# Kernel tuning notes

Hardware: AMD Instinct MI355X
Metric: run time of the kernel (lower is better)

## Reference

```python
import jax, jax.numpy as jnp
import numpy as np

K = 8        # num_heads
D = 32       # out_dim per head
KD = K * D   # 256
IN = 256     # in_dim
N_AUTHOR = 50000
N_PAPER = 50000
E = 400000
SLOPE = 0.2  # LeakyReLU negative slope


def setup_inputs() -> dict:
    key = jax.random.key(0)
    ks = jax.random.split(key, 26)
    f32 = jnp.float32
    nrm = lambda k, shp, s=0.05: jax.random.normal(k, shp, f32) * s
    ridx = lambda k, n: jax.random.randint(k, (E,), 0, n, jnp.int32)
    return {
        # node features
        "feats_author": nrm(ks[0], (N_AUTHOR, IN), 1.0),
        "feats_paper": nrm(ks[1], (N_PAPER, IN), 1.0),
        # micro (per node type) projection + attention vectors
        "W_micro_author": nrm(ks[2], (IN, KD)),
        "W_micro_paper": nrm(ks[3], (IN, KD)),
        "attn_micro_author": nrm(ks[4], (K, 2 * D)),
        "attn_micro_paper": nrm(ks[5], (K, 2 * D)),
        # macro: node projection per ntype, relation projection per etype
        "W_macro_node_author": nrm(ks[6], (IN, KD)),
        "W_macro_node_paper": nrm(ks[7], (IN, KD)),
        "W_macro_rel_writes": nrm(ks[8], (KD, KD)),
        "W_macro_rel_written_by": nrm(ks[9], (KD, KD)),
        "W_macro_rel_cites": nrm(ks[10], (KD, KD)),
        "attn_macro": nrm(ks[11], (K, 2 * D)),
        # residual
        "W_res_author": nrm(ks[12], (IN, KD)),
        "b_res_author": jnp.zeros((KD,), f32),
        "W_res_paper": nrm(ks[13], (IN, KD)),
        "b_res_paper": jnp.zeros((KD,), f32),
        "res_w_author": jax.random.uniform(ks[14], (1,), f32),
        "res_w_paper": jax.random.uniform(ks[15], (1,), f32),
        # graph: author-writes->paper, paper-written_by->author, paper-cites->paper
        "writes_src": ridx(ks[16], N_AUTHOR),
        "writes_dst": ridx(ks[17], N_PAPER),
        "written_by_src": ridx(ks[18], N_PAPER),
        "written_by_dst": ridx(ks[19], N_AUTHOR),
        "cites_src": ridx(ks[20], N_PAPER),
        "cites_dst": ridx(ks[21], N_PAPER),
    }


def _edge_softmax(e, dst, n_dst):
    # softmax over incoming edges of each destination node; e: (E, K)
    m = jax.ops.segment_max(e, dst, num_segments=n_dst)
    ex = jnp.exp(e - m[dst])
    s = jax.ops.segment_sum(ex, dst, num_segments=n_dst)
    return ex / s[dst]


def _micro(h_src, h_dst, W_s, W_d, attn, src, dst, n_dst):
    # GAT-style per-relation message passing (MicroConv, dropout=0 eval)
    fs = (h_src @ W_s).reshape(-1, K, D)   # (N_src, K, D)
    fd = (h_dst @ W_d).reshape(-1, K, D)   # (N_dst, K, D)
    el = (fs * attn[:, :D]).sum(-1)        # (N_src, K)
    er = (fd * attn[:, D:]).sum(-1)        # (N_dst, K)
    e = jax.nn.leaky_relu(el[src] + er[dst], SLOPE)  # (E, K)
    a = _edge_softmax(e, dst, n_dst)
    ft = jax.ops.segment_sum(fs[src] * a[:, :, None], dst, num_segments=n_dst)
    return jax.nn.relu(ft.reshape(n_dst, KD))


def reference(feats_author, feats_paper, W_micro_author, W_micro_paper,
              attn_micro_author, attn_micro_paper, W_macro_node_author,
              W_macro_node_paper, W_macro_rel_writes, W_macro_rel_written_by,
              W_macro_rel_cites, attn_macro, W_res_author, b_res_author,
              W_res_paper, b_res_paper, res_w_author, res_w_paper,
              writes_src, writes_dst, written_by_src, written_by_dst,
              cites_src, cites_dst):
    # --- micro conv per relation; fc_src/fc_dst keyed by node type, attn by src type ---
    r_writes = _micro(feats_author, feats_paper, W_micro_author, W_micro_paper,
                      attn_micro_author, writes_src, writes_dst, N_PAPER)
    r_written_by = _micro(feats_paper, feats_author, W_micro_paper, W_micro_author,
                          attn_micro_paper, written_by_src, written_by_dst, N_AUTHOR)
    r_cites = _micro(feats_paper, feats_paper, W_micro_paper, W_micro_paper,
                     attn_micro_paper, cites_src, cites_dst, N_PAPER)

    # --- macro conv: relation-level projection ---
    rf_writes = (r_writes @ W_macro_rel_writes).reshape(-1, K, D)
    rf_written_by = (r_written_by @ W_macro_rel_written_by).reshape(-1, K, D)
    rf_cites = (r_cites @ W_macro_rel_cites).reshape(-1, K, D)

    # author: single incoming relation -> passthrough
    out_author = rf_written_by.reshape(-1, KD)

    # paper: two incoming relations -> semantic attention fusion
    node_paper = (feats_paper @ W_macro_node_paper).reshape(-1, K, D)
    rf = jnp.stack([rf_writes, rf_cites], axis=0)          # (R=2, N, K, D)
    node_b = jnp.broadcast_to(node_paper, rf.shape)
    cat = jnp.concatenate([node_b, rf], axis=-1)           # (R, N, K, 2D)
    scores = jax.nn.leaky_relu((attn_macro * cat).sum(-1, keepdims=True), SLOPE)
    scores = jax.nn.softmax(scores, axis=0)                # over relations
    out_paper = (scores * rf).sum(0).reshape(-1, KD)

    # --- gated residual ---
    a_a = jax.nn.sigmoid(res_w_author)
    a_p = jax.nn.sigmoid(res_w_paper)
    out_author = a_a * out_author + (1 - a_a) * (feats_author @ W_res_author + b_res_author)
    out_paper = a_p * out_paper + (1 - a_p) * (feats_paper @ W_res_paper + b_res_paper)
    return out_author, out_paper
```

## Files before the change

kernel.cpp:

```cpp
#include <hip/hip_runtime.h>
#include <hip/hip_bf16.h>
#include <type_traits>


#define N_AUTHOR 50000
#define N_PAPER  50000
#define NEDGE    400000
#define KDIM     256
#define NHEAD    8
#define SLOPE    0.2f

#define BUCK_W   512
#define NBUCK    98
#define SBUF_CAP 6144

#define CSR_STRIDE 450004
#define CSR_GSRC   50004

using bf16 = __hip_bfloat16;
typedef __attribute__((ext_vector_type(8))) short short8;
typedef __attribute__((ext_vector_type(4))) float float4e;

__device__ __forceinline__ float us2f(unsigned short u) {
    return __uint_as_float(((unsigned int)u) << 16);
}
__device__ __forceinline__ float fin(float v) {
    return (((__float_as_uint(v) >> 23) & 0xFF) != 0xFF) ? v : 0.f;
}
__device__ __forceinline__ unsigned short f2bu(float f) {
    f = fin(f);
    bf16 h = __float2bfloat16(f);
    return *reinterpret_cast<unsigned short*>(&h);
}
__device__ __forceinline__ int clampi(int v, int hi) {
    return v < 0 ? 0 : (v >= hi ? hi - 1 : v);
}

__global__ void fill_marker(float* __restrict__ out, int total, float c)
{
    int i = blockIdx.x * blockDim.x + threadIdx.x;
    if (i < total) out[i] = c;
}

__device__ __forceinline__ float sel8(const float p[8], int j)
{
    float q = p[0];
    q = j == 1 ? p[1] : q; q = j == 2 ? p[2] : q; q = j == 3 ? p[3] : q;
    q = j == 4 ? p[4] : q; q = j == 5 ? p[5] : q; q = j == 6 ? p[6] : q;
    q = j == 7 ? p[7] : q;
    return q;
}

__device__ __forceinline__ float head_reduce(float p[8], int lane)
{
    #pragma unroll
    for (int h = 0; h < 8; ++h) {
        p[h] += __shfl_xor(p[h], 1);
        p[h] += __shfl_xor(p[h], 2);
        p[h] += __shfl_xor(p[h], 4);
    }
    float q = sel8(p, lane & 7);
    q += __shfl_xor(q, 8);
    q += __shfl_xor(q, 16);
    q += __shfl_xor(q, 32);
    return q;
}

__global__ void prep_bt(const float* __restrict__ W, bf16* __restrict__ BT)
{
    int n = blockIdx.x, k = threadIdx.x;
    reinterpret_cast<unsigned short*>(BT)[n * KDIM + k] = f2bu(W[k * KDIM + n]);
}

template<int MODE, typename TA>
__global__ __launch_bounds__(256) void mfma_gemm(
    const TA* __restrict__ A, const bf16* __restrict__ BT, int M,
    void* __restrict__ Cout,
    const float* __restrict__ bias, const bf16* __restrict__ other,
    const float* __restrict__ gate,
    const bf16* __restrict__ rfw, const float* __restrict__ sc_w,
    const float* __restrict__ sc_c)
{
    __shared__ short As[128 * 40];
    __shared__ short Bs[128 * 40];
    const int tid = threadIdx.x;
    const int lane = tid & 63, wave = tid >> 6;
    const int wm = wave >> 1, wn = wave & 1;
    const int rowBase = blockIdx.y * 128;
    const int colBase = blockIdx.x * 128;

    float4e acc[4][4];
    #pragma unroll
    for (int i = 0; i < 4; ++i)
        #pragma unroll
        for (int j = 0; j < 4; ++j) {
            float4e z = {0.f, 0.f, 0.f, 0.f};
            acc[i][j] = z;
        }

    const int srow = tid >> 2;
    const int sq = (tid & 3) << 3;

    for (int kt = 0; kt < KDIM; kt += 32) {
        #pragma unroll
        for (int p = 0; p < 2; ++p) {
            int r = srow + p * 64;
            int gr = rowBase + r;
            short8 v = {0, 0, 0, 0, 0, 0, 0, 0};
            if (gr < M) {
                if constexpr (std::is_same<TA, float>::value) {
                    const float* ap = A + (size_t)gr * KDIM + kt + sq;
                    float4 x = *reinterpret_cast<const float4*>(ap);
                    float4 y = *reinterpret_cast<const float4*>(ap + 4);
                    v[0] = (short)f2bu(x.x); v[1] = (short)f2bu(x.y);
                    v[2] = (short)f2bu(x.z); v[3] = (short)f2bu(x.w);
                    v[4] = (short)f2bu(y.x); v[5] = (short)f2bu(y.y);
                    v[6] = (short)f2bu(y.z); v[7] = (short)f2bu(y.w);
                } else {
                    v = *reinterpret_cast<const short8*>(
                        reinterpret_cast<const short*>(A) + (size_t)gr * KDIM + kt + sq);
                }
            }
            *reinterpret_cast<short8*>(&As[r * 40 + sq]) = v;
        }
        #pragma unroll
        for (int p = 0; p < 2; ++p) {
            int n = srow + p * 64;
            short8 v = *reinterpret_cast<const short8*>(
                reinterpret_cast<const short*>(BT) + (size_t)(colBase + n) * KDIM + kt + sq);
            *reinterpret_cast<short8*>(&Bs[n * 40 + sq]) = v;
        }
        __syncthreads();

        short8 af[4], bg[4];
        #pragma unroll
        for (int i = 0; i < 4; ++i)
            af[i] = *reinterpret_cast<const short8*>(
                &As[(wm * 64 + i * 16 + (lane & 15)) * 40 + ((lane >> 4) << 3)]);
        #pragma unroll
        for (int j = 0; j < 4; ++j)
            bg[j] = *reinterpret_cast<const short8*>(
                &Bs[(wn * 64 + j * 16 + (lane & 15)) * 40 + ((lane >> 4) << 3)]);
        #pragma unroll
        for (int i = 0; i < 4; ++i)
            #pragma unroll
            for (int j = 0; j < 4; ++j)
                acc[i][j] = __builtin_amdgcn_mfma_f32_16x16x32_bf16(
                    af[i], bg[j], acc[i][j], 0, 0, 0);
        __syncthreads();
    }

    float al = 0.f;
    if constexpr (MODE == 2) al = 1.f / (1.f + expf(-gate[0]));

    #pragma unroll
    for (int i = 0; i < 4; ++i) {
        int r0 = rowBase + wm * 64 + i * 16 + ((lane >> 4) << 2);
        #pragma unroll
        for (int j = 0; j < 4; ++j) {
            int col = colBase + wn * 64 + j * 16 + (lane & 15);
            #pragma unroll
            for (int reg = 0; reg < 4; ++reg) {
                int row = r0 + reg;
                if (row < M) {
                    size_t idx = (size_t)row * KDIM + col;
                    float v = acc[i][j][reg];
                    if constexpr (MODE == 0) {
                        reinterpret_cast<unsigned short*>(Cout)[idx] = f2bu(v);
                    } else if constexpr (MODE == 1) {
                        int h = col >> 5;
                        size_t si = (size_t)row * NHEAD + h;
                        float f = sc_w[si] * us2f(reinterpret_cast<const unsigned short*>(rfw)[idx])
                                + sc_c[si] * v;
                        reinterpret_cast<unsigned short*>(Cout)[idx] = f2bu(f);
                    } else {
                        float of = us2f(reinterpret_cast<const unsigned short*>(other)[idx]);
                        reinterpret_cast<float*>(Cout)[idx] =
                            fin(al * of + (1.f - al) * (v + bias[col]));
                    }
                }
            }
        }
    }
}

__global__ void head_dot2(const bf16* __restrict__ proj,
                          const float* __restrict__ aA, int offA, float* __restrict__ oA,
                          const float* __restrict__ aB, int offB, float* __restrict__ oB,
                          int N)
{
    int gid = blockIdx.x * blockDim.x + threadIdx.x;
    if (gid >= N * NHEAD) return;
    int n = gid >> 3, k = gid & 7;
    const unsigned short* p =
        reinterpret_cast<const unsigned short*>(proj) + (size_t)n * KDIM + k * 32;
    const float* a = aA + k * 64 + offA;
    const float* b = aB + k * 64 + offB;
    float sA = 0.f, sB = 0.f;
    #pragma unroll
    for (int d0 = 0; d0 < 32; d0 += 4) {
        ushort4 pv = *reinterpret_cast<const ushort4*>(p + d0);
        float4 av = *reinterpret_cast<const float4*>(a + d0);
        float4 bv = *reinterpret_cast<const float4*>(b + d0);
        float f0 = us2f(pv.x), f1 = us2f(pv.y), f2 = us2f(pv.z), f3 = us2f(pv.w);
        sA += f0 * av.x + f1 * av.y + f2 * av.z + f3 * av.w;
        sB += f0 * bv.x + f1 * bv.y + f2 * bv.z + f3 * bv.w;
    }
    oA[gid] = fin(sA);
    oB[gid] = fin(sB);
}

__global__ void head_dot3(const bf16* __restrict__ proj,
                          const float* __restrict__ aA, int offA, float* __restrict__ oA,
                          const float* __restrict__ aB, int offB, float* __restrict__ oB,
                          const float* __restrict__ aC, int offC, float* __restrict__ oC,
                          int N)
{
    int gid = blockIdx.x * blockDim.x + threadIdx.x;
    if (gid >= N * NHEAD) return;
    int n = gid >> 3, k = gid & 7;
    const unsigned short* p =
        reinterpret_cast<const unsigned short*>(proj) + (size_t)n * KDIM + k * 32;
    const float* a = aA + k * 64 + offA;
    const float* b = aB + k * 64 + offB;
    const float* c = aC + k * 64 + offC;
    float sA = 0.f, sB = 0.f, sC = 0.f;
    #pragma unroll
    for (int d0 = 0; d0 < 32; d0 += 4) {
        ushort4 pv = *reinterpret_cast<const ushort4*>(p + d0);
        float4 av = *reinterpret_cast<const float4*>(a + d0);
        float4 bv = *reinterpret_cast<const float4*>(b + d0);
        float4 cv = *reinterpret_cast<const float4*>(c + d0);
        float f0 = us2f(pv.x), f1 = us2f(pv.y), f2 = us2f(pv.z), f3 = us2f(pv.w);
        sA += f0 * av.x + f1 * av.y + f2 * av.z + f3 * av.w;
        sB += f0 * bv.x + f1 * bv.y + f2 * bv.z + f3 * bv.w;
        sC += f0 * cv.x + f1 * cv.y + f2 * cv.z + f3 * cv.w;
    }
    oA[gid] = fin(sA);
    oB[gid] = fin(sB);
    oC[gid] = fin(sC);
}

__global__ void zero_meta(int* __restrict__ meta)
{
    int i = threadIdx.x + blockIdx.x * blockDim.x;
    if (i < 3 * NBUCK) meta[i] = 0;
    if (i < 3 * NBUCK) meta[591 + i] = 0;
}

__global__ __launch_bounds__(256) void bucket_count(
    const int* __restrict__ d0, const int* __restrict__ d1,
    const int* __restrict__ d2, int* __restrict__ meta, int E)
{
    __shared__ int cnt[NBUCK];
    for (int i = threadIdx.x; i < NBUCK; i += 256) cnt[i] = 0;
    __syncthreads();
    int r = blockIdx.y;
    const int* d = r == 0 ? d0 : (r == 1 ? d1 : d2);
    for (int e = blockIdx.x * 256 + threadIdx.x; e < E; e += gridDim.x * 256)
        atomicAdd(&cnt[clampi(d[e], N_PAPER) >> 9], 1);
    __syncthreads();
    for (int i = threadIdx.x; i < NBUCK; i += 256)
        if (cnt[i]) atomicAdd(&meta[r * NBUCK + i], cnt[i]);
}

__global__ void bucket_scan(int* __restrict__ meta)
{
    int r = threadIdx.x >> 6, lane = threadIdx.x & 63;
    if (r >= 3) return;
    const int* gbcnt = meta + r * NBUCK;
    int* bbase = meta + 294 + r * (NBUCK + 1);
    int carry = 0;
    for (int base = 0; base < NBUCK; base += 64) {
        int i = base + lane;
        int v = (i < NBUCK) ? gbcnt[i] : 0;
        int x = v;
        #pragma unroll
        for (int o = 1; o < 64; o <<= 1) {
            int t = __shfl_up(x, o, 64);
            if (lane >= o) x += t;
        }
        if (i < NBUCK) bbase[i] = carry + x - v;
        carry += __shfl(x, 63, 64);
    }
    if (lane == 0) bbase[NBUCK] = carry;
}

__global__ __launch_bounds__(256) void bucket_scatter(
    const int* __restrict__ s0, const int* __restrict__ s1,
    const int* __restrict__ s2,
    const int* __restrict__ d0, const int* __restrict__ d1,
    const int* __restrict__ d2,
    int* __restrict__ meta, int* __restrict__ T, int E)
{
    __shared__ int cnt[NBUCK];
    __shared__ int base[NBUCK];
    int r = blockIdx.y;
    const int* s = r == 0 ? s0 : (r == 1 ? s1 : s2);
    const int* d = r == 0 ? d0 : (r == 1 ? d1 : d2);
    const int* bbase = meta + 294 + r * (NBUCK + 1);
    int* grank = meta + 591 + r * NBUCK;
    int* Tr = T + r * NEDGE;

    for (int i = threadIdx.x; i < NBUCK; i += 256) cnt[i] = 0;
    __syncthreads();

    const int CH = (E + gridDim.x - 1) / gridDim.x;
    int e0 = blockIdx.x * CH;
    int e1 = min(e0 + CH, E);
    for (int e = e0 + threadIdx.x; e < e1; e += 256)
        atomicAdd(&cnt[clampi(d[e], N_PAPER) >> 9], 1);
    __syncthreads();
    if (threadIdx.x < NBUCK) {
        int c = cnt[threadIdx.x];
        base[threadIdx.x] = c ? bbase[threadIdx.x] + atomicAdd(&grank[threadIdx.x], c) : 0;
        cnt[threadIdx.x] = 0;
    }
    __syncthreads();
    for (int e = e0 + threadIdx.x; e < e1; e += 256) {
        int dc = clampi(d[e], N_PAPER);
        int b = dc >> 9, dl = dc & 511;
        int l = atomicAdd(&cnt[b], 1);
        Tr[base[b] + l] = (clampi(s[e], N_PAPER) << 9) | dl;
    }
}

__global__ __launch_bounds__(256) void csr_build(
    const int* __restrict__ meta, const int* __restrict__ T,
    int* __restrict__ csr)
{
    __shared__ int cnt[512];
    __shared__ int loc[512];
    __shared__ int sbuf[SBUF_CAP];
    __shared__ int wtot[4];
    int b = blockIdx.x, r = blockIdx.y;
    const int* bbase = meta + 294 + r * (NBUCK + 1);
    const int* Tr = T + r * NEDGE;
    int* off = csr + r * CSR_STRIDE;
    int* gsrc = off + CSR_GSRC;
    const int tid = threadIdx.x, lane = tid & 63, wv = tid >> 6;

    int dstbase = b << 9;
    int nd = min(512, N_PAPER - dstbase);
    int cbase = bbase[b], cend = bbase[b + 1];
    int span = cend - cbase;

    cnt[2 * tid] = 0; cnt[2 * tid + 1] = 0;
    __syncthreads();
    for (int t = tid; t < span; t += 256)
        atomicAdd(&cnt[Tr[cbase + t] & 511], 1);
    __syncthreads();

    int v0 = cnt[2 * tid], v1 = cnt[2 * tid + 1];
    int sthr = v0 + v1;
    int x = sthr;
    #pragma unroll
    for (int o = 1; o < 64; o <<= 1) {
        int t = __shfl_up(x, o, 64);
        if (lane >= o) x += t;
    }
    if (lane == 63) wtot[wv] = x;
    __syncthreads();
    int wexc = 0;
    #pragma unroll
    for (int w = 0; w < 4; ++w)
        if (w < wv) wexc += wtot[w];
    int exc = wexc + x - sthr;
    loc[2 * tid] = exc;
    loc[2 * tid + 1] = exc + v0;
    int i0 = 2 * tid, i1 = 2 * tid + 1;
    if (i0 < nd) off[dstbase + i0] = cbase + exc;
    if (i1 < nd) off[dstbase + i1] = cbase + exc + v0;
    if (b == NBUCK - 1 && tid == 0) off[N_PAPER] = cend;
    cnt[i0] = 0; cnt[i1] = 0;
    __syncthreads();

    if (span <= SBUF_CAP) {
        for (int t = tid; t < span; t += 256) {
            int v = Tr[cbase + t];
            int dl = v & 511;
            int pos = loc[dl] + atomicAdd(&cnt[dl], 1);
            sbuf[pos] = v >> 9;
        }
        __syncthreads();
        for (int t = tid; t < span; t += 256)
            gsrc[cbase + t] = sbuf[t];
    } else {
        for (int t = tid; t < span; t += 256) {
            int v = Tr[cbase + t];
            int dl = v & 511;
            int pos = loc[dl] + atomicAdd(&cnt[dl], 1);
            gsrc[cbase + pos] = v >> 9;
        }
    }
}

__global__ __launch_bounds__(256) void gat_gather(
    const int* __restrict__ off, const int* __restrict__ gsrc,
    const float* __restrict__ el, const float* __restrict__ er,
    const bf16* __restrict__ feat, bf16* __restrict__ out,
    const float* __restrict__ dv, float* __restrict__ dout, int N)
{
    __shared__ float vlds[2048];
    if (dv) {
        #pragma unroll
        for (int i = 0; i < 2; ++i) {
            int idx = (i * 256 + threadIdx.x) * 4;
            *reinterpret_cast<float4*>(&vlds[idx]) =
                *reinterpret_cast<const float4*>(&dv[idx]);
        }
        __syncthreads();
    }
    int d = blockIdx.x * 4 + (threadIdx.x >> 6);
    if (d >= N) return;
    int lane = threadIdx.x & 63;
    int hL = lane >> 3;
    int col = lane * 4;
    int ep = lane >> 3, hM = lane & 7;
    float erdM = er[d * NHEAD + hM];
    int e0 = off[d], e1 = off[d + 1];
    float denom = 0.f, a0 = 0.f, a1 = 0.f, a2 = 0.f, a3 = 0.f;
    for (int e = e0; e < e1; e += 8) {
        int nc = e1 - e; nc = nc > 8 ? 8 : nc;
        int sM = 0; float exM = 0.f;
        if (ep < nc) {
            sM = gsrc[e + ep];
            float v = el[sM * NHEAD + hM] + erdM;
            v = v > 0.f ? v : SLOPE * v;
            exM = expf(fminf(v, 30.f));
        }
        #pragma unroll
        for (int q = 0; q < 8; ++q) {
            if (q < nc) {
                float ex = __shfl(exM, q * 8 + hL);
                int s = __shfl(sM, q * 8);
                denom += ex;
                ushort4 fv = *reinterpret_cast<const ushort4*>(
                    reinterpret_cast<const unsigned short*>(feat) + (size_t)s * KDIM + col);
                a0 = fmaf(us2f(fv.x), ex, a0); a1 = fmaf(us2f(fv.y), ex, a1);
                a2 = fmaf(us2f(fv.z), ex, a2); a3 = fmaf(us2f(fv.w), ex, a3);
            }
        }
    }
    float inv = 1.f / fmaxf(denom, 1e-20f);
    float o0 = fmaxf(a0 * inv, 0.f), o1 = fmaxf(a1 * inv, 0.f);
    float o2 = fmaxf(a2 * inv, 0.f), o3 = fmaxf(a3 * inv, 0.f);
    ushort4 o;
    o.x = f2bu(o0); o.y = f2bu(o1); o.z = f2bu(o2); o.w = f2bu(o3);
    *reinterpret_cast<ushort4*>(
        reinterpret_cast<unsigned short*>(out) + (size_t)d * KDIM + col) = o;
    if (dv) {
        float p[8];
        #pragma unroll
        for (int hh = 0; hh < 8; ++hh) {
            float4 vv = *reinterpret_cast<const float4*>(&vlds[hh * 256 + col]);
            p[hh] = o0 * vv.x + o1 * vv.y + o2 * vv.z + o3 * vv.w;
        }
        float q = head_reduce(p, lane);
        if (lane < 8) dout[d * NHEAD + lane] = fin(q);
    }
}

__global__ void prep_v(const float* __restrict__ Ww, const float* __restrict__ Wc,
                       const float* __restrict__ Wn, const float* __restrict__ attn,
                       float* __restrict__ vbuf)
{
    int id = blockIdx.x * blockDim.x + threadIdx.x;
    if (id >= 3 * 2048) return;
    int which = id >> 11;
    int rem = id & 2047;
    int h = rem >> 8, k = rem & 255;
    const float* Wsrc = which == 0 ? Ww : (which == 1 ? Wc : Wn);
    int aoff = which == 2 ? 0 : 32;
    float s = 0.f;
    #pragma unroll 8
    for (int d = 0; d < 32; ++d)
        s += Wsrc[(size_t)k * KDIM + h * 32 + d] * attn[h * 64 + aoff + d];
    vbuf[which * 2048 + h * 256 + k] = fin(s);
}

__global__ __launch_bounds__(256) void macro_dotL(
    const float* __restrict__ Af, const float* __restrict__ vL,
    float* __restrict__ dout, int N)
{
    __shared__ float vlds[2048];
    #pragma unroll
    for (int i = 0; i < 2; ++i) {
        int idx = (i * 256 + threadIdx.x) * 4;
        *reinterpret_cast<float4*>(&vlds[idx]) =
            *reinterpret_cast<const float4*>(&vL[idx]);
    }
    __syncthreads();
    int n = blockIdx.x * 4 + (threadIdx.x >> 6);
    if (n >= N) return;
    int lane = threadIdx.x & 63;
    int col = lane * 4;
    float4e afv = __builtin_nontemporal_load(
        reinterpret_cast<const float4e*>(Af + (size_t)n * KDIM + col));
    float p[8];
    #pragma unroll
    for (int h = 0; h < 8; ++h) {
        float4 vv = *reinterpret_cast<const float4*>(&vlds[h * 256 + col]);
        p[h] = afv.x * vv.x + afv.y * vv.y + afv.z * vv.z + afv.w * vv.w;
    }
    float q = head_reduce(p, lane);
    if (lane < 8) dout[n * NHEAD + lane] = fin(q);
}

__global__ void score_kernel(const float* __restrict__ dotL, const float* __restrict__ dotW,
                             const float* __restrict__ dotC,
                             float* __restrict__ ow, float* __restrict__ oc, int total)
{
    int i = blockIdx.x * blockDim.x + threadIdx.x;
    if (i >= total) return;
    float sw = dotL[i] + dotW[i]; sw = sw > 0.f ? sw : SLOPE * sw;
    float sc = dotL[i] + dotC[i]; sc = sc > 0.f ? sc : SLOPE * sc;
    float m = fmaxf(sw, sc);
    float ew = expf(sw - m), ec = expf(sc - m);
    float inv = 1.f / (ew + ec);
    ow[i] = fin(ew * inv);
    oc[i] = fin(ec * inv);
}

extern "C" void kernel_launch(void* const* d_in, const int* in_sizes, int n_in,
                              void* d_out, int out_size, void* d_ws, size_t ws_size,
                              hipStream_t stream)
{
    static const int expected[24] = {
        12800000, 12800000, 65536, 65536, 512, 512, 65536, 65536,
        65536, 65536, 65536, 512, 65536, 256, 65536, 256, 1, 1,
        400000, 400000, 400000, 400000, 400000, 400000};
    float marker = 0.f;
    if (n_in != 24) marker = 500.f;
    else {
        for (int i = 0; i < 24; ++i)
            if (in_sizes[i] != expected[i]) { marker = 200.f + 8.f * i; break; }
    }
    if (marker == 0.f && out_size != 25600000) marker = 600.f + (float)(out_size / 1000000);
    if (marker == 0.f && ws_size < 51200000ull) marker = 1000.f + (float)(ws_size / 1000000ull);
    if (marker != 0.f) {
        fill_marker<<<(out_size + 255) / 256, 256, 0, stream>>>((float*)d_out, out_size, marker);
        return;
    }

    const float* feats_a  = (const float*)d_in[0];
    const float* feats_p  = (const float*)d_in[1];
    const float* W_mic_a  = (const float*)d_in[2];
    const float* W_mic_p  = (const float*)d_in[3];
    const float* attn_a   = (const float*)d_in[4];
    const float* attn_p   = (const float*)d_in[5];
    const float* W_node_p = (const float*)d_in[7];
    const float* W_rel_w  = (const float*)d_in[8];
    const float* W_rel_wb = (const float*)d_in[9];
    const float* W_rel_c  = (const float*)d_in[10];
    const float* attn_mac = (const float*)d_in[11];
    const float* W_res_a  = (const float*)d_in[12];
    const float* b_res_a  = (const float*)d_in[13];
    const float* W_res_p  = (const float*)d_in[14];
    const float* b_res_p  = (const float*)d_in[15];
    const float* rw_a     = (const float*)d_in[16];
    const float* rw_p     = (const float*)d_in[17];
    const int* w_src  = (const int*)d_in[18];
    const int* w_dst  = (const int*)d_in[19];
    const int* wb_src = (const int*)d_in[20];
    const int* wb_dst = (const int*)d_in[21];
    const int* c_src  = (const int*)d_in[22];
    const int* c_dst  = (const int*)d_in[23];

    const int NB = N_PAPER * KDIM;
    float* Oa_f = (float*)d_out;
    float* Op_f = Oa_f + NB;
    bf16* Oa_b = (bf16*)d_out;
    bf16* Op_b = (bf16*)Op_f;
    char* au_up = (char*)d_out + 25600000;
    bf16*  Cslot = (bf16*)au_up;
    bf16*  BTa0  = (bf16*)au_up;
    bf16*  BTa1  = BTa0 + 65536;
    char* pu = (char*)d_out + 76800000;
    float* dotW = (float*)pu;
    float* dotC = dotW + 400000;
    float* dotL = dotW + 800000;
    float* sc_w = dotW + 1200000;
    float* sc_c = dotW + 1600000;
    float* vbuf = dotW + 2000000;
    bf16* BT0 = (bf16*)(pu + 10000000);
    bf16* BT1 = BT0 + 65536;
    bf16* BT2 = BT1 + 65536;
    bf16* BT3 = BT2 + 65536;
    bf16* A_ws = (bf16*)d_ws;
    bf16* BTw  = (bf16*)d_ws;
    char* Xb   = (char*)d_ws + 25600000;
    float* el_w  = (float*)Xb;
    float* er_w  = el_w + 400000;
    float* el_p  = el_w + 800000;
    float* er_wb = el_w + 1200000;
    float* er_c  = el_w + 1600000;
    int*  csr    = (int*)(el_w + 2000000);
    int*  Tbuf   = csr + 3 * CSR_STRIDE;
    int*  meta   = Tbuf + 3 * NEDGE;
    bf16* Xslot  = (bf16*)Xb;

    dim3 mg(2, (N_PAPER + 127) / 128);
    int hdB = (N_PAPER * NHEAD + 255) / 256;
    int gB  = (N_PAPER + 3) / 4;

    prep_bt<<<256, 256, 0, stream>>>(W_mic_a, BT0);
    prep_bt<<<256, 256, 0, stream>>>(W_mic_p, BT1);
    mfma_gemm<0, float><<<mg, 256, 0, stream>>>(feats_a, BT0, N_AUTHOR, Oa_b,
        nullptr, nullptr, nullptr, nullptr, nullptr, nullptr);
    mfma_gemm<0, float><<<mg, 256, 0, stream>>>(feats_p, BT1, N_PAPER, Op_b,
        nullptr, nullptr, nullptr, nullptr, nullptr, nullptr);

    head_dot2<<<hdB, 256, 0, stream>>>(Oa_b, attn_a, 0, el_w,
                                       attn_p, 32, er_wb, N_AUTHOR);
    head_dot3<<<hdB, 256, 0, stream>>>(Op_b, attn_a, 32, er_w,
                                       attn_p, 0, el_p,
                                       attn_p, 32, er_c, N_PAPER);

    zero_meta<<<2, 256, 0, stream>>>(meta);
    bucket_count<<<dim3(64, 3), 256, 0, stream>>>(w_dst, wb_dst, c_dst, meta, NEDGE);
    bucket_scan<<<1, 192, 0, stream>>>(meta);
    bucket_scatter<<<dim3(64, 3), 256, 0, stream>>>(w_src, wb_src, c_src,
                                                    w_dst, wb_dst, c_dst,
                                                    meta, Tbuf, NEDGE);
    csr_build<<<dim3(NBUCK, 3), 256, 0, stream>>>(meta, Tbuf, csr);
    prep_v<<<24, 256, 0, stream>>>(W_rel_w, W_rel_c, W_node_p, attn_mac, vbuf);
    {
        const float* rel_el[3] = {el_w, el_p, el_p};
        const float* rel_er[3] = {er_w, er_wb, er_c};
        const bf16* rfeat[3]   = {Oa_b, Op_b, Op_b};
        bf16* rout[3]          = {A_ws, Oa_b, Cslot};
        const float* rdv[3]    = {vbuf, nullptr, vbuf + 2048};
        float* rdo[3]          = {dotW, nullptr, dotC};
        for (int r = 0; r < 3; ++r) {
            int* off  = csr + r * CSR_STRIDE;
            int* gsrc = off + CSR_GSRC;
            gat_gather<<<gB, 256, 0, stream>>>(off, gsrc, rel_el[r], rel_er[r],
                                               rfeat[r], rout[r],
                                               rdv[r], rdo[r], N_PAPER);
        }
    }

    macro_dotL<<<gB, 256, 0, stream>>>(feats_p, vbuf + 4096, dotL, N_PAPER);
    score_kernel<<<hdB, 256, 0, stream>>>(dotL, dotW, dotC, sc_w, sc_c, N_PAPER * NHEAD);

    prep_bt<<<256, 256, 0, stream>>>(W_rel_w, BT2);
    mfma_gemm<0, bf16><<<mg, 256, 0, stream>>>(A_ws, BT2, N_PAPER, Op_b,
        nullptr, nullptr, nullptr, nullptr, nullptr, nullptr);
    prep_bt<<<256, 256, 0, stream>>>(W_rel_c, BT3);
    mfma_gemm<1, bf16><<<mg, 256, 0, stream>>>(Cslot, BT3, N_PAPER, A_ws,
        nullptr, nullptr, nullptr, Op_b, sc_w, sc_c);
    prep_bt<<<256, 256, 0, stream>>>(W_res_p, BTa0);
    mfma_gemm<2, float><<<mg, 256, 0, stream>>>(feats_p, BTa0, N_PAPER, Op_f,
        b_res_p, A_ws, rw_p, nullptr, nullptr, nullptr);
    prep_bt<<<256, 256, 0, stream>>>(W_rel_wb, BTa1);
    mfma_gemm<0, bf16><<<mg, 256, 0, stream>>>(Oa_b, BTa1, N_AUTHOR, Xslot,
        nullptr, nullptr, nullptr, nullptr, nullptr, nullptr);
    prep_bt<<<256, 256, 0, stream>>>(W_res_a, BTw);
    mfma_gemm<2, float><<<mg, 256, 0, stream>>>(feats_a, BTw, N_AUTHOR, Oa_f,
        b_res_a, Xslot, rw_a, nullptr, nullptr, nullptr);
}
```

Measured before the change: 812.2 us.

## Fuse paper macro GEMMs and residual into one kernel with full-width row tiles

Replaces the 128x128-tile GEMM with 64-row by 256-column tiles, so each block covers a full output row and the A operand is read once. The three paper-side GEMMs (writes relation, cites relation, residual) are fused into one kernel that keeps the accumulators in registers and applies the semantic softmax weights and the gated residual before a single fp32 write. This removes the bf16 intermediate round-trips through global memory and two kernel launches. The cost is more registers (two accumulator sets, which can lower occupancy) and a larger LDS tile for B.

```diff
diff --git a/kernel.cpp b/kernel.cpp
--- a/kernel.cpp
+++ b/kernel.cpp
@@ -72,24 +72,13 @@
     reinterpret_cast<unsigned short*>(BT)[n * KDIM + k] = f2bu(W[k * KDIM + n]);
 }
 
-template<int MODE, typename TA>
-__global__ __launch_bounds__(256) void mfma_gemm(
-    const TA* __restrict__ A, const bf16* __restrict__ BT, int M,
-    void* __restrict__ Cout,
-    const float* __restrict__ bias, const bf16* __restrict__ other,
-    const float* __restrict__ gate,
-    const bf16* __restrict__ rfw, const float* __restrict__ sc_w,
-    const float* __restrict__ sc_c)
-{
-    __shared__ short As[128 * 40];
-    __shared__ short Bs[128 * 40];
-    const int tid = threadIdx.x;
-    const int lane = tid & 63, wave = tid >> 6;
-    const int wm = wave >> 1, wn = wave & 1;
-    const int rowBase = blockIdx.y * 128;
-    const int colBase = blockIdx.x * 128;
-
-    float4e acc[4][4];
+template<typename TA>
+__device__ __forceinline__ void gemm_pass(
+    const TA* __restrict__ A, const bf16* __restrict__ BT, int M, int rowBase,
+    short* As, short* Bs, float4e acc[4][4], int tid, int lane, int wn)
+{
+    const int srow = tid >> 2;
+    const int sq = (tid & 3) << 3;
     #pragma unroll
     for (int i = 0; i < 4; ++i)
         #pragma unroll
@@ -97,15 +86,9 @@
             float4e z = {0.f, 0.f, 0.f, 0.f};
             acc[i][j] = z;
         }
-
-    const int srow = tid >> 2;
-    const int sq = (tid & 3) << 3;
-
     for (int kt = 0; kt < KDIM; kt += 32) {
-        #pragma unroll
-        for (int p = 0; p < 2; ++p) {
-            int r = srow + p * 64;
-            int gr = rowBase + r;
+        {
+            int gr = rowBase + srow;
             short8 v = {0, 0, 0, 0, 0, 0, 0, 0};
             if (gr < M) {
                 if constexpr (std::is_same<TA, float>::value) {
@@ -121,22 +104,21 @@
                         reinterpret_cast<const short*>(A) + (size_t)gr * KDIM + kt + sq);
                 }
             }
-            *reinterpret_cast<short8*>(&As[r * 40 + sq]) = v;
-        }
-        #pragma unroll
-        for (int p = 0; p < 2; ++p) {
+            *reinterpret_cast<short8*>(&As[srow * 40 + sq]) = v;
+        }
+        #pragma unroll
+        for (int p = 0; p < 4; ++p) {
             int n = srow + p * 64;
             short8 v = *reinterpret_cast<const short8*>(
-                reinterpret_cast<const short*>(BT) + (size_t)(colBase + n) * KDIM + kt + sq);
+                reinterpret_cast<const short*>(BT) + (size_t)n * KDIM + kt + sq);
             *reinterpret_cast<short8*>(&Bs[n * 40 + sq]) = v;
         }
         __syncthreads();
-
         short8 af[4], bg[4];
         #pragma unroll
         for (int i = 0; i < 4; ++i)
             af[i] = *reinterpret_cast<const short8*>(
-                &As[(wm * 64 + i * 16 + (lane & 15)) * 40 + ((lane >> 4) << 3)]);
+                &As[(i * 16 + (lane & 15)) * 40 + ((lane >> 4) << 3)]);
         #pragma unroll
         for (int j = 0; j < 4; ++j)
             bg[j] = *reinterpret_cast<const short8*>(
@@ -149,35 +131,112 @@
                     af[i], bg[j], acc[i][j], 0, 0, 0);
         __syncthreads();
     }
-
-    float al = 0.f;
-    if constexpr (MODE == 2) al = 1.f / (1.f + expf(-gate[0]));
-
+}
+
+template<typename TA>
+__global__ __launch_bounds__(256) void gemm_c16(
+    const TA* __restrict__ A, const bf16* __restrict__ BT, int M,
+    bf16* __restrict__ C)
+{
+    __shared__ short As[64 * 40];
+    __shared__ short Bs[256 * 40];
+    const int tid = threadIdx.x, lane = tid & 63, wn = tid >> 6;
+    const int rowBase = blockIdx.x * 64;
+    float4e acc[4][4];
+    gemm_pass(A, BT, M, rowBase, As, Bs, acc, tid, lane, wn);
     #pragma unroll
     for (int i = 0; i < 4; ++i) {
-        int r0 = rowBase + wm * 64 + i * 16 + ((lane >> 4) << 2);
+        int r0 = rowBase + i * 16 + ((lane >> 4) << 2);
         #pragma unroll
         for (int j = 0; j < 4; ++j) {
-            int col = colBase + wn * 64 + j * 16 + (lane & 15);
+            int col = wn * 64 + j * 16 + (lane & 15);
+            #pragma unroll
+            for (int reg = 0; reg < 4; ++reg) {
+                int row = r0 + reg;
+                if (row < M)
+                    reinterpret_cast<unsigned short*>(C)[(size_t)row * KDIM + col] =
+                        f2bu(acc[i][j][reg]);
+            }
+        }
+    }
+}
+
+__global__ __launch_bounds__(256) void gemm_paper(
+    const bf16* __restrict__ A1, const bf16* __restrict__ BT1,
+    const bf16* __restrict__ A2, const bf16* __restrict__ BT2,
+    const float* __restrict__ A3, const bf16* __restrict__ BT3, int M,
+    const float* __restrict__ sc_w, const float* __restrict__ sc_c,
+    const float* __restrict__ gate, const float* __restrict__ bias,
+    float* __restrict__ C)
+{
+    __shared__ short As[64 * 40];
+    __shared__ short Bs[256 * 40];
+    const int tid = threadIdx.x, lane = tid & 63, wn = tid >> 6;
+    const int rowBase = blockIdx.x * 64;
+    float4e accA[4][4], accB[4][4];
+    gemm_pass(A1, BT1, M, rowBase, As, Bs, accA, tid, lane, wn);
+    gemm_pass(A2, BT2, M, rowBase, As, Bs, accB, tid, lane, wn);
+    #pragma unroll
+    for (int i = 0; i < 4; ++i) {
+        int r0 = rowBase + i * 16 + ((lane >> 4) << 2);
+        #pragma unroll
+        for (int j = 0; j < 4; ++j) {
+            int h = (wn * 64 + j * 16 + (lane & 15)) >> 5;
+            #pragma unroll
+            for (int reg = 0; reg < 4; ++reg) {
+                int row = r0 + reg;
+                int rc = row < M ? row : M - 1;
+                size_t si = (size_t)rc * NHEAD + h;
+                accA[i][j][reg] = sc_w[si] * accA[i][j][reg]
+                                + sc_c[si] * accB[i][j][reg];
+            }
+        }
+    }
+    gemm_pass(A3, BT3, M, rowBase, As, Bs, accB, tid, lane, wn);
+    float al = 1.f / (1.f + expf(-gate[0]));
+    #pragma unroll
+    for (int i = 0; i < 4; ++i) {
+        int r0 = rowBase + i * 16 + ((lane >> 4) << 2);
+        #pragma unroll
+        for (int j = 0; j < 4; ++j) {
+            int col = wn * 64 + j * 16 + (lane & 15);
+            #pragma unroll
+            for (int reg = 0; reg < 4; ++reg) {
+                int row = r0 + reg;
+                if (row < M)
+                    C[(size_t)row * KDIM + col] =
+                        fin(al * accA[i][j][reg]
+                            + (1.f - al) * (accB[i][j][reg] + bias[col]));
+            }
+        }
+    }
+}
+
+__global__ __launch_bounds__(256) void gemm_resid(
+    const float* __restrict__ A, const bf16* __restrict__ BT, int M,
+    const bf16* __restrict__ other, const float* __restrict__ gate,
+    const float* __restrict__ bias, float* __restrict__ C)
+{
+    __shared__ short As[64 * 40];
+    __shared__ short Bs[256 * 40];
+    const int tid = threadIdx.x, lane = tid & 63, wn = tid >> 6;
+    const int rowBase = blockIdx.x * 64;
+    float4e acc[4][4];
+    gemm_pass(A, BT, M, rowBase, As, Bs, acc, tid, lane, wn);
+    float al = 1.f / (1.f + expf(-gate[0]));
+    #pragma unroll
+    for (int i = 0; i < 4; ++i) {
+        int r0 = rowBase + i * 16 + ((lane >> 4) << 2);
+        #pragma unroll
+        for (int j = 0; j < 4; ++j) {
+            int col = wn * 64 + j * 16 + (lane & 15);
             #pragma unroll
             for (int reg = 0; reg < 4; ++reg) {
                 int row = r0 + reg;
                 if (row < M) {
                     size_t idx = (size_t)row * KDIM + col;
-                    float v = acc[i][j][reg];
-                    if constexpr (MODE == 0) {
-                        reinterpret_cast<unsigned short*>(Cout)[idx] = f2bu(v);
-                    } else if constexpr (MODE == 1) {
-                        int h = col >> 5;
-                        size_t si = (size_t)row * NHEAD + h;
-                        float f = sc_w[si] * us2f(reinterpret_cast<const unsigned short*>(rfw)[idx])
-                                + sc_c[si] * v;
-                        reinterpret_cast<unsigned short*>(Cout)[idx] = f2bu(f);
-                    } else {
-                        float of = us2f(reinterpret_cast<const unsigned short*>(other)[idx]);
-                        reinterpret_cast<float*>(Cout)[idx] =
-                            fin(al * of + (1.f - al) * (v + bias[col]));
-                    }
+                    float of = us2f(reinterpret_cast<const unsigned short*>(other)[idx]);
+                    C[idx] = fin(al * of + (1.f - al) * (acc[i][j][reg] + bias[col]));
                 }
             }
         }
@@ -574,21 +633,14 @@
     bf16* Op_b = (bf16*)Op_f;
     char* au_up = (char*)d_out + 25600000;
     bf16*  Cslot = (bf16*)au_up;
-    bf16*  BTa0  = (bf16*)au_up;
-    bf16*  BTa1  = BTa0 + 65536;
     char* pu = (char*)d_out + 76800000;
     float* dotW = (float*)pu;
     float* dotC = dotW + 400000;
     float* dotL = dotW + 800000;
-    float* sc_w = dotW + 1200000;
-    float* sc_c = dotW + 1600000;
-    float* vbuf = dotW + 2000000;
+    float* vbuf = dotW + 1200000;
     bf16* BT0 = (bf16*)(pu + 10000000);
     bf16* BT1 = BT0 + 65536;
-    bf16* BT2 = BT1 + 65536;
-    bf16* BT3 = BT2 + 65536;
     bf16* A_ws = (bf16*)d_ws;
-    bf16* BTw  = (bf16*)d_ws;
     char* Xb   = (char*)d_ws + 25600000;
     float* el_w  = (float*)Xb;
     float* er_w  = el_w + 400000;
@@ -598,18 +650,22 @@
     int*  csr    = (int*)(el_w + 2000000);
     int*  Tbuf   = csr + 3 * CSR_STRIDE;
     int*  meta   = Tbuf + 3 * NEDGE;
-    bf16* Xslot  = (bf16*)Xb;
-
-    dim3 mg(2, (N_PAPER + 127) / 128);
+    float* sc_w = (float*)Xb;
+    float* sc_c = sc_w + 400000;
+    bf16* BT2 = (bf16*)(Xb + 8000000);
+    bf16* BT3 = BT2 + 65536;
+    bf16* BT4 = BT3 + 65536;
+    bf16* BT5 = BT4 + 65536;
+    bf16* BT6 = BT5 + 65536;
+
+    int gemB = (N_PAPER + 63) / 64;
     int hdB = (N_PAPER * NHEAD + 255) / 256;
     int gB  = (N_PAPER + 3) / 4;
 
     prep_bt<<<256, 256, 0, stream>>>(W_mic_a, BT0);
     prep_bt<<<256, 256, 0, stream>>>(W_mic_p, BT1);
-    mfma_gemm<0, float><<<mg, 256, 0, stream>>>(feats_a, BT0, N_AUTHOR, Oa_b,
-        nullptr, nullptr, nullptr, nullptr, nullptr, nullptr);
-    mfma_gemm<0, float><<<mg, 256, 0, stream>>>(feats_p, BT1, N_PAPER, Op_b,
-        nullptr, nullptr, nullptr, nullptr, nullptr, nullptr);
+    gemm_c16<float><<<gemB, 256, 0, stream>>>(feats_a, BT0, N_AUTHOR, Oa_b);
+    gemm_c16<float><<<gemB, 256, 0, stream>>>(feats_p, BT1, N_PAPER, Op_b);
 
     head_dot2<<<hdB, 256, 0, stream>>>(Oa_b, attn_a, 0, el_w,
                                        attn_p, 32, er_wb, N_AUTHOR);
@@ -641,22 +697,17 @@
         }
     }
 
+    prep_bt<<<256, 256, 0, stream>>>(W_rel_w,  BT2);
+    prep_bt<<<256, 256, 0, stream>>>(W_rel_c,  BT3);
+    prep_bt<<<256, 256, 0, stream>>>(W_res_p,  BT4);
+    prep_bt<<<256, 256, 0, stream>>>(W_rel_wb, BT5);
+    prep_bt<<<256, 256, 0, stream>>>(W_res_a,  BT6);
     macro_dotL<<<gB, 256, 0, stream>>>(feats_p, vbuf + 4096, dotL, N_PAPER);
     score_kernel<<<hdB, 256, 0, stream>>>(dotL, dotW, dotC, sc_w, sc_c, N_PAPER * NHEAD);
 
-    prep_bt<<<256, 256, 0, stream>>>(W_rel_w, BT2);
-    mfma_gemm<0, bf16><<<mg, 256, 0, stream>>>(A_ws, BT2, N_PAPER, Op_b,
-        nullptr, nullptr, nullptr, nullptr, nullptr, nullptr);
-    prep_bt<<<256, 256, 0, stream>>>(W_rel_c, BT3);
-    mfma_gemm<1, bf16><<<mg, 256, 0, stream>>>(Cslot, BT3, N_PAPER, A_ws,
-        nullptr, nullptr, nullptr, Op_b, sc_w, sc_c);
-    prep_bt<<<256, 256, 0, stream>>>(W_res_p, BTa0);
-    mfma_gemm<2, float><<<mg, 256, 0, stream>>>(feats_p, BTa0, N_PAPER, Op_f,
-        b_res_p, A_ws, rw_p, nullptr, nullptr, nullptr);
-    prep_bt<<<256, 256, 0, stream>>>(W_rel_wb, BTa1);
-    mfma_gemm<0, bf16><<<mg, 256, 0, stream>>>(Oa_b, BTa1, N_AUTHOR, Xslot,
-        nullptr, nullptr, nullptr, nullptr, nullptr, nullptr);
-    prep_bt<<<256, 256, 0, stream>>>(W_res_a, BTw);
-    mfma_gemm<2, float><<<mg, 256, 0, stream>>>(feats_a, BTw, N_AUTHOR, Oa_f,
-        b_res_a, Xslot, rw_a, nullptr, nullptr, nullptr);
-}
+    gemm_paper<<<gemB, 256, 0, stream>>>(A_ws, BT2, Cslot, BT3, feats_p, BT4,
+                                         N_PAPER, sc_w, sc_c, rw_p, b_res_p, Op_f);
+    gemm_c16<bf16><<<gemB, 256, 0, stream>>>(Oa_b, BT5, N_AUTHOR, A_ws);
+    gemm_resid<<<gemB, 256, 0, stream>>>(feats_a, BT6, N_AUTHOR, A_ws,
+                                         rw_a, b_res_a, Oa_f);
+}
```

New measurement: 771.3 us. -5.0%, faster.
